# Kernel tuning notes

Hardware: AMD Instinct MI355X
Metric: run time of the kernel (lower is better)

Reference implementation:

```python
import jax, jax.numpy as jnp
import numpy as np

N_HEADS = 16
D_HEAD = 64
IGNORE = -100000.0


def setup_inputs() -> dict:
    key = jax.random.key(0)
    ks = jax.random.split(key, 5)
    B, S, D = 2, 2048, 1024
    return {
        "residual": jax.random.normal(ks[0], (B, S, D), dtype=jnp.float32),
        "q": jax.random.normal(ks[1], (B, S, D), dtype=jnp.float32),
        "k": jax.random.normal(ks[2], (B, S, D), dtype=jnp.float32),
        "v": jax.random.normal(ks[3], (B, S, D), dtype=jnp.float32),
        "W_O": jax.random.normal(ks[4], (N_HEADS, D_HEAD, D), dtype=jnp.float32) * 0.02,
        "b_O": jnp.zeros((D,), dtype=jnp.float32),
    }


def reference(residual, q, k, v, W_O, b_O):
    B, S, _ = q.shape
    attn_scale = np.sqrt(D_HEAD).astype(np.float32)  # use_attn_scale=True
    # split heads: [..., pos, (h d)] -> [..., pos, h, d]
    qh = q.reshape(B, S, N_HEADS, D_HEAD)
    kh = k.reshape(B, S, N_HEADS, D_HEAD)
    vh = v.reshape(B, S, N_HEADS, D_HEAD)
    # scores: [..., head, query_pos, key_pos]
    scores = jnp.einsum("bqhd,bkhd->bhqk", qh, kh) / attn_scale
    causal = jnp.tril(jnp.ones((S, S), dtype=bool))
    scores = jnp.where(causal, scores, jnp.float32(IGNORE))
    pattern = jax.nn.softmax(scores, axis=-1)
    # weighted sum of values: [..., query_pos, head, d_head]
    z = jnp.einsum("bkhd,bhqk->bqhd", vh, pattern)
    out = jnp.einsum("bqhd,hdm->bqm", z, W_O) + b_O
    return (residual, out)
```

## Files before the change

kernel.cpp:

```cpp
#include <hip/hip_runtime.h>

#define B_ 2
#define S_ 2048
#define D_ 1024
#define H_ 16
#define DH_ 64
#define NP_ 2048

typedef short v8s __attribute__((ext_vector_type(8)));
typedef float v4f __attribute__((ext_vector_type(4)));
typedef float v16f __attribute__((ext_vector_type(16)));
typedef unsigned int v2u __attribute__((ext_vector_type(2)));
typedef unsigned int v4u __attribute__((ext_vector_type(4)));
typedef unsigned int uint32;

__device__ inline short f2bf(float f) {
  unsigned u = __float_as_uint(f);
  u = (u + 0x7FFFu + ((u >> 16) & 1u)) >> 16;
  return (short)u;
}

__device__ inline unsigned pk_bf16(float lo, float hi) {
  unsigned r;
  asm("v_cvt_pk_bf16_f32 %0, %1, %2" : "=v"(r) : "v"(lo), "v"(hi));
  return r;
}

__device__ inline void gll16(const void* g, void* l) {
  __builtin_amdgcn_global_load_lds(
      (const __attribute__((address_space(1))) void*)g,
      (__attribute__((address_space(3))) void*)l, 16, 0, 0);
}

__global__ __launch_bounds__(256) void cvt_bf16_kernel(const float* __restrict__ in,
                                                       short* __restrict__ out) {
  int i = blockIdx.x * blockDim.x + threadIdx.x;
  float4 a = ((const float4*)in)[2 * i];
  float4 b = ((const float4*)in)[2 * i + 1];
  v8s t;
  t[0] = f2bf(a.x); t[1] = f2bf(a.y); t[2] = f2bf(a.z); t[3] = f2bf(a.w);
  t[4] = f2bf(b.x); t[5] = f2bf(b.y); t[6] = f2bf(b.z); t[7] = f2bf(b.w);
  ((v8s*)out)[i] = t;
}

__global__ __launch_bounds__(256) void cvt_vt_kernel(const float* __restrict__ v,
                                                     short* __restrict__ vt) {
  int bid = blockIdx.x;
  int st = bid & 31;
  int bh = bid >> 5;
  int b = bh >> 4, h = bh & 15;
  int tid = threadIdx.x;
  __shared__ short t[64][64 + 8];
  int r = tid >> 2, c16 = (tid & 3) * 16;
  const float* vp = v + ((size_t)(b * S_ + st * 64 + r)) * D_ + h * DH_ + c16;
  for (int i = 0; i < 16; i += 4) {
    float4 a = *(const float4*)(vp + i);
    t[r][c16 + i + 0] = f2bf(a.x);
    t[r][c16 + i + 1] = f2bf(a.y);
    t[r][c16 + i + 2] = f2bf(a.z);
    t[r][c16 + i + 3] = f2bf(a.w);
  }
  __syncthreads();
  short* op = vt + ((size_t)((b * H_ + h) * DH_ + r)) * S_ + st * 64 + c16;
  v8s o0, o1;
  for (int j = 0; j < 8; ++j) { o0[j] = t[c16 + j][r]; o1[j] = t[c16 + 8 + j][r]; }
  *(v8s*)op = o0;
  *(v8s*)(op + 8) = o1;
}

__global__ __launch_bounds__(256) void cvt_wt_kernel(const float* __restrict__ w,
                                                     short* __restrict__ wt) {
  int bid = blockIdx.x;
  int tk = bid & 15, tm = bid >> 4;
  int tid = threadIdx.x;
  __shared__ short t[64][64 + 8];
  int r = tid >> 2, c16 = (tid & 3) * 16;
  const float* wp = w + (size_t)(tk * 64 + r) * D_ + tm * 64 + c16;
  for (int i = 0; i < 16; i += 4) {
    float4 a = *(const float4*)(wp + i);
    t[r][c16 + i + 0] = f2bf(a.x);
    t[r][c16 + i + 1] = f2bf(a.y);
    t[r][c16 + i + 2] = f2bf(a.z);
    t[r][c16 + i + 3] = f2bf(a.w);
  }
  __syncthreads();
  short* op = wt + (size_t)(tm * 64 + r) * D_ + tk * 64 + c16;
  v8s o0, o1;
  for (int j = 0; j < 8; ++j) { o0[j] = t[c16 + j][r]; o1[j] = t[c16 + 8 + j][r]; }
  *(v8s*)op = o0;
  *(v8s*)(op + 8) = o1;
}

template <int SPLITS>
__global__ __launch_bounds__(128, 4) void attn_kernel(
    const float* __restrict__ q, const short* __restrict__ kbf,
    const short* __restrict__ vtb, uint32* __restrict__ Opart,
    float* __restrict__ Lsum) {
  constexpr int SHIFT = (SPLITS == 2 ? 6 : 5);
  int bid = blockIdx.x;
  int bh = bid & 31;
  int sp = (SPLITS == 2) ? ((bid >> 5) & 1) : 0;
  int qt = 31 - (int)(bid >> SHIFT);
  int b = bh >> 4, h = bh & 15;

  int nt = qt + 1;
  int hs = (nt + 1) >> 1;
  int t0 = (SPLITS == 2 && sp == 1) ? hs : 0;
  int t1 = (SPLITS == 2 && sp == 0) ? hs - 1 : qt;

  int tid = threadIdx.x;
  int wave = tid >> 6, lane = tid & 63;
  int l31 = lane & 31, h32 = lane >> 5;

  __shared__ short Klds[64][64];
  __shared__ short Vlds[64][64];

  const int qrow0 = qt * 64 + wave * 32;
  const int lr8 = lane >> 3;
  const int scol = ((lane & 7) ^ lr8) << 3;

  const short* pk_ = kbf + (size_t)b * S_ * D_ + h * DH_ +
                     (size_t)(t0 * 64 + wave * 8 + lr8) * D_ + scol;
  const short* pv_ = vtb + (size_t)(b * H_ + h) * DH_ * S_ +
                     (size_t)(wave * 8 + lr8) * S_ + t0 * 64 + scol;

  v8s qf[4];
  {
    const float* qp = q + (size_t)(b * S_ + qrow0 + l31) * D_ + h * DH_ + h32 * 8;
    const float sc = 0.125f * 1.44269504f;
#pragma unroll
    for (int d4 = 0; d4 < 4; ++d4) {
      float4 x = *(const float4*)(qp + d4 * 16);
      float4 y = *(const float4*)(qp + d4 * 16 + 4);
      v8s tq;
      tq[0] = f2bf(x.x * sc); tq[1] = f2bf(x.y * sc);
      tq[2] = f2bf(x.z * sc); tq[3] = f2bf(x.w * sc);
      tq[4] = f2bf(y.x * sc); tq[5] = f2bf(y.y * sc);
      tq[6] = f2bf(y.z * sc); tq[7] = f2bf(y.w * sc);
      qf[d4] = tq;
    }
  }

  v16f O0, O1;
#pragma unroll
  for (int r = 0; r < 16; ++r) { O0[r] = 0.f; O1[r] = 0.f; }
  float L = 0.f;
  const int swz = (l31 & 7) << 3;

  for (int s = t0; s <= t1; ++s) {
#pragma unroll
    for (int i = 0; i < 4; ++i)
      gll16(pk_ + (size_t)(i * 16) * D_, &Klds[i * 16 + wave * 8][0]);
#pragma unroll
    for (int i = 0; i < 4; ++i)
      gll16(pv_ + (size_t)(i * 16) * S_, &Vlds[i * 16 + wave * 8][0]);
    pk_ += (size_t)64 * D_;
    pv_ += 64;
    asm volatile("s_waitcnt vmcnt(0)" ::: "memory");
    __builtin_amdgcn_sched_barrier(0);
    __builtin_amdgcn_s_barrier();
    __builtin_amdgcn_sched_barrier(0);

    int kb = s * 64;
    bool skip1 = (kb >= qrow0);
    bool msk = (kb + 63 > qrow0);

    __builtin_amdgcn_s_setprio(1);
    v16f S0, S1;
#pragma unroll
    for (int r = 0; r < 16; ++r) { S0[r] = 0.f; S1[r] = 0.f; }
#pragma unroll
    for (int d4 = 0; d4 < 4; ++d4) {
      v8s kf = *(const v8s*)&Klds[l31][(((d4 << 1) | h32) << 3) ^ swz];
      S0 = __builtin_amdgcn_mfma_f32_32x32x16_bf16(kf, qf[d4], S0, 0, 0, 0);
    }
    if (!skip1) {
#pragma unroll
      for (int d4 = 0; d4 < 4; ++d4) {
        v8s kf = *(const v8s*)&Klds[32 + l31][(((d4 << 1) | h32) << 3) ^ swz];
        S1 = __builtin_amdgcn_mfma_f32_32x32x16_bf16(kf, qf[d4], S1, 0, 0, 0);
      }
    }
    __builtin_amdgcn_s_setprio(0);

    int qg = qrow0 + l31;
    if (msk) {
#pragma unroll
      for (int r = 0; r < 16; ++r) {
        int kl = kb + (r & 3) + 8 * (r >> 2) + 4 * h32;
        if (kl > qg) S0[r] = -1e30f;
      }
      if (!skip1) {
#pragma unroll
        for (int r = 0; r < 16; ++r) {
          int kl = kb + 32 + (r & 3) + 8 * (r >> 2) + 4 * h32;
          if (kl > qg) S1[r] = -1e30f;
        }
      }
    }

    float rs = 0.f;
    unsigned pw0[8], pw1[8];
#pragma unroll
    for (int r = 0; r < 16; ++r) {
      S0[r] = __builtin_amdgcn_exp2f(S0[r]);
      rs += S0[r];
    }
#pragma unroll
    for (int w = 0; w < 8; ++w) pw0[w] = pk_bf16(S0[2 * w], S0[2 * w + 1]);
    if (!skip1) {
#pragma unroll
      for (int r = 0; r < 16; ++r) {
        S1[r] = __builtin_amdgcn_exp2f(S1[r]);
        rs += S1[r];
      }
#pragma unroll
      for (int w = 0; w < 8; ++w) pw1[w] = pk_bf16(S1[2 * w], S1[2 * w + 1]);
    }
    rs += __shfl_xor(rs, 32);
    L += rs;

    __builtin_amdgcn_s_setprio(1);
#pragma unroll
    for (int ks = 0; ks < 2; ++ks) {
      v2u a = __builtin_amdgcn_permlane32_swap(pw0[ks * 4 + 0], pw0[ks * 4 + 2], false, false);
      v2u c = __builtin_amdgcn_permlane32_swap(pw0[ks * 4 + 1], pw0[ks * 4 + 3], false, false);
      v4u fw; fw.x = a.x; fw.y = c.x; fw.z = a.y; fw.w = c.y;
      v8s pb = __builtin_bit_cast(v8s, fw);
      v8s vf0 = *(const v8s*)&Vlds[l31][(((ks << 1) | h32) << 3) ^ swz];
      O0 = __builtin_amdgcn_mfma_f32_32x32x16_bf16(vf0, pb, O0, 0, 0, 0);
      v8s vf1 = *(const v8s*)&Vlds[32 + l31][(((ks << 1) | h32) << 3) ^ swz];
      O1 = __builtin_amdgcn_mfma_f32_32x32x16_bf16(vf1, pb, O1, 0, 0, 0);
    }
    if (!skip1) {
#pragma unroll
      for (int ks = 0; ks < 2; ++ks) {
        v2u a = __builtin_amdgcn_permlane32_swap(pw1[ks * 4 + 0], pw1[ks * 4 + 2], false, false);
        v2u c = __builtin_amdgcn_permlane32_swap(pw1[ks * 4 + 1], pw1[ks * 4 + 3], false, false);
        v4u fw; fw.x = a.x; fw.y = c.x; fw.z = a.y; fw.w = c.y;
        v8s pb = __builtin_bit_cast(v8s, fw);
        v8s vf0 = *(const v8s*)&Vlds[l31][((((ks + 2) << 1) | h32) << 3) ^ swz];
        O0 = __builtin_amdgcn_mfma_f32_32x32x16_bf16(vf0, pb, O0, 0, 0, 0);
        v8s vf1 = *(const v8s*)&Vlds[32 + l31][((((ks + 2) << 1) | h32) << 3) ^ swz];
        O1 = __builtin_amdgcn_mfma_f32_32x32x16_bf16(vf1, pb, O1, 0, 0, 0);
      }
    }
    __builtin_amdgcn_s_setprio(0);

    __builtin_amdgcn_sched_barrier(0);
    __builtin_amdgcn_s_barrier();
    __builtin_amdgcn_sched_barrier(0);
  }

  int p = bh * 64 + qt * 2 + wave;
  uint32* Op = Opart + ((size_t)(sp * NP_ + p)) * 1024;
#pragma unroll
  for (int w = 0; w < 8; ++w) {
    int dpair = 4 * (w >> 1) + (w & 1) + 2 * h32;
    Op[dpair * 32 + l31] = pk_bf16(O0[2 * w], O0[2 * w + 1]);
    Op[(16 + dpair) * 32 + l31] = pk_bf16(O1[2 * w], O1[2 * w + 1]);
  }
  if (h32 == 0) Lsum[(size_t)(sp * NP_ + p) * 32 + l31] = L;
}

template <int SPLITS>
__global__ __launch_bounds__(128) void merge_kernel(
    const uint32* __restrict__ Opart, const float* __restrict__ Lsum,
    short* __restrict__ z) {
  int p = blockIdx.x;
  int tid = threadIdx.x;
  int qq = tid & 31, g = tid >> 5;

  float Lt = Lsum[(size_t)p * 32 + qq];
  if constexpr (SPLITS == 2) Lt += Lsum[(size_t)(NP_ + p) * 32 + qq];
  float f = 1.f / Lt;

  __shared__ uint32 T[32][33];
  const uint32* O0 = Opart + (size_t)p * 1024;
  const uint32* O1 = Opart + (size_t)(NP_ + p) * 1024;
#pragma unroll
  for (int j = 0; j < 8; ++j) {
    int dp = g * 8 + j;
    uint32 u0 = O0[dp * 32 + qq];
    float lo = __uint_as_float(u0 << 16);
    float hi = __uint_as_float(u0 & 0xFFFF0000u);
    if constexpr (SPLITS == 2) {
      uint32 u1 = O1[dp * 32 + qq];
      lo += __uint_as_float(u1 << 16);
      hi += __uint_as_float(u1 & 0xFFFF0000u);
    }
    T[qq][dp] = pk_bf16(lo * f, hi * f);
  }
  __syncthreads();
  int q2 = tid >> 2, c = (tid & 3) * 8;
  int srow = (p & 63) * 32 + q2;
  int b = p >> 10, h = (p >> 6) & 15;
  uint32* zp = (uint32*)z + ((size_t)(b * S_ + srow)) * (D_ / 2) + h * 32 + c;
#pragma unroll
  for (int j = 0; j < 8; ++j) zp[j] = T[q2][c + j];
}

__global__ __launch_bounds__(256) void proj_kernel(
    const short* __restrict__ z, const short* __restrict__ wt,
    const float* __restrict__ bias, float* __restrict__ out) {
  int bm = blockIdx.x, bn = blockIdx.y;
  int tid = threadIdx.x;
  int wave = tid >> 6, lane = tid & 63, lh = lane >> 4, ll = lane & 15;
  int wr = wave >> 1, wc = wave & 1;

  __shared__ short Al[2][64][64];
  __shared__ short Bl[2][128][64];

  const int r8 = lane >> 3;
  const int scol = ((lane & 7) ^ r8) << 3;

  v4f acc[2][4];
#pragma unroll
  for (int m = 0; m < 2; ++m)
#pragma unroll
    for (int n = 0; n < 4; ++n) acc[m][n] = (v4f){0.f, 0.f, 0.f, 0.f};

  auto stage = [&](int kb, int bbuf) {
#pragma unroll
    for (int i = 0; i < 2; ++i) {
      int c = wave * 2 + i;
      gll16(z + (size_t)(bm * 64 + c * 8 + r8) * D_ + kb + scol, &Al[bbuf][c * 8][0]);
    }
#pragma unroll
    for (int i = 0; i < 4; ++i) {
      int c = wave * 4 + i;
      gll16(wt + (size_t)(bn * 128 + c * 8 + r8) * D_ + kb + scol, &Bl[bbuf][c * 8][0]);
    }
  };

  stage(0, 0);
  __syncthreads();

  for (int kt = 0; kt < D_ / 64; ++kt) {
    int bbuf = kt & 1;
    if (kt + 1 < D_ / 64) stage((kt + 1) * 64, bbuf ^ 1);
    v8s af[2][2], bf[4][2];
#pragma unroll
    for (int m = 0; m < 2; ++m) {
      int row = wr * 32 + m * 16 + ll;
#pragma unroll
      for (int c = 0; c < 2; ++c)
        af[m][c] = *(const v8s*)&Al[bbuf][row][(((c << 2) | lh) ^ (ll & 7)) << 3];
    }
#pragma unroll
    for (int n = 0; n < 4; ++n) {
      int row = wc * 64 + n * 16 + ll;
#pragma unroll
      for (int c = 0; c < 2; ++c)
        bf[n][c] = *(const v8s*)&Bl[bbuf][row][(((c << 2) | lh) ^ (ll & 7)) << 3];
    }
#pragma unroll
    for (int m = 0; m < 2; ++m)
#pragma unroll
      for (int n = 0; n < 4; ++n)
#pragma unroll
        for (int c = 0; c < 2; ++c)
          acc[m][n] = __builtin_amdgcn_mfma_f32_16x16x32_bf16(af[m][c], bf[n][c], acc[m][n], 0, 0, 0);
    __syncthreads();
  }

#pragma unroll
  for (int m = 0; m < 2; ++m) {
    int gr = bm * 64 + wr * 32 + m * 16 + lh * 4;
#pragma unroll
    for (int n = 0; n < 4; ++n) {
      int gc = bn * 128 + wc * 64 + n * 16 + ll;
      float bo = bias[gc];
#pragma unroll
      for (int r = 0; r < 4; ++r)
        out[(size_t)(gr + r) * D_ + gc] = acc[m][n][r] + bo;
    }
  }
}

extern "C" void kernel_launch(void* const* d_in, const int* in_sizes, int n_in,
                              void* d_out, int out_size, void* d_ws, size_t ws_size,
                              hipStream_t stream) {
  const float* residual = (const float*)d_in[0];
  const float* q = (const float*)d_in[1];
  const float* k = (const float*)d_in[2];
  const float* v = (const float*)d_in[3];
  const float* W = (const float*)d_in[4];
  const float* bO = (const float*)d_in[5];
  float* out = (float*)d_out;

  const size_t half = (size_t)B_ * S_ * D_;
  char* ws = (char*)d_ws;
  short* z = (short*)ws;
  short* kbf = z + half;
  short* vtb = kbf + half;
  short* wtb = vtb + half;
  char* pbase = (char*)(wtb + (size_t)D_ * D_);
  const size_t opart_b = (size_t)NP_ * 1024 * 4;
  const size_t l_b = (size_t)NP_ * 32 * 4;
  const size_t base_b = (size_t)pbase - (size_t)ws;

  hipMemcpyAsync(out, residual, half * sizeof(float), hipMemcpyDeviceToDevice, stream);

  cvt_bf16_kernel<<<half / 2048, 256, 0, stream>>>(k, kbf);
  cvt_vt_kernel<<<B_ * H_ * (S_ / 64), 256, 0, stream>>>(v, vtb);
  cvt_wt_kernel<<<(D_ / 64) * (D_ / 64), 256, 0, stream>>>(W, wtb);

  if (ws_size >= base_b + 2 * (opart_b + l_b)) {
    uint32* Opart = (uint32*)pbase;
    float* Lsum = (float*)(pbase + 2 * opart_b);
    attn_kernel<2><<<2048, 128, 0, stream>>>(q, kbf, vtb, Opart, Lsum);
    merge_kernel<2><<<NP_, 128, 0, stream>>>(Opart, Lsum, z);
  } else {
    uint32* Opart = (uint32*)pbase;
    float* Lsum = (float*)(pbase + opart_b);
    attn_kernel<1><<<1024, 128, 0, stream>>>(q, kbf, vtb, Opart, Lsum);
    merge_kernel<1><<<NP_, 128, 0, stream>>>(Opart, Lsum, z);
  }

  proj_kernel<<<dim3((B_ * S_) / 64, D_ / 128), 256, 0, stream>>>(z, wtb, bO, out + half);
}
```

Before: 77.09 us.

## Fuse conversions, balance causal split-K by tile length, fold residual copy into attention

Merges the three bf16 conversion kernels into one launch. Splits causal query tiles into 1–4 key chunks depending on tile length, so every attention block handles a similar amount of work, and the merge reduces a variable number of partials. Moves the residual memcpy into the tail of the attention kernel as a grid-stride copy, and reuses the K buffer for z to save workspace. This cuts launch count and tail imbalance, but adds more partial-buffer traffic and workspace.

```diff
diff --git a/kernel.cpp b/kernel.cpp
--- a/kernel.cpp
+++ b/kernel.cpp
@@ -32,81 +32,88 @@
       (__attribute__((address_space(3))) void*)l, 16, 0, 0);
 }
 
-__global__ __launch_bounds__(256) void cvt_bf16_kernel(const float* __restrict__ in,
-                                                       short* __restrict__ out) {
-  int i = blockIdx.x * blockDim.x + threadIdx.x;
-  float4 a = ((const float4*)in)[2 * i];
-  float4 b = ((const float4*)in)[2 * i + 1];
-  v8s t;
-  t[0] = f2bf(a.x); t[1] = f2bf(a.y); t[2] = f2bf(a.z); t[3] = f2bf(a.w);
-  t[4] = f2bf(b.x); t[5] = f2bf(b.y); t[6] = f2bf(b.z); t[7] = f2bf(b.w);
-  ((v8s*)out)[i] = t;
-}
-
-__global__ __launch_bounds__(256) void cvt_vt_kernel(const float* __restrict__ v,
-                                                     short* __restrict__ vt) {
+__global__ __launch_bounds__(256) void cvt_all_kernel(
+    const float* __restrict__ k, short* __restrict__ kb,
+    const float* __restrict__ v, short* __restrict__ vt,
+    const float* __restrict__ w, short* __restrict__ wt) {
+  __shared__ short t[64][64 + 8];
   int bid = blockIdx.x;
-  int st = bid & 31;
-  int bh = bid >> 5;
-  int b = bh >> 4, h = bh & 15;
   int tid = threadIdx.x;
-  __shared__ short t[64][64 + 8];
+  if (bid < 2048) {
+    int i = bid * 256 + tid;
+    float4 a = ((const float4*)k)[2 * i];
+    float4 b = ((const float4*)k)[2 * i + 1];
+    v8s o;
+    o[0] = f2bf(a.x); o[1] = f2bf(a.y); o[2] = f2bf(a.z); o[3] = f2bf(a.w);
+    o[4] = f2bf(b.x); o[5] = f2bf(b.y); o[6] = f2bf(b.z); o[7] = f2bf(b.w);
+    ((v8s*)kb)[i] = o;
+    return;
+  }
   int r = tid >> 2, c16 = (tid & 3) * 16;
-  const float* vp = v + ((size_t)(b * S_ + st * 64 + r)) * D_ + h * DH_ + c16;
-  for (int i = 0; i < 16; i += 4) {
-    float4 a = *(const float4*)(vp + i);
-    t[r][c16 + i + 0] = f2bf(a.x);
-    t[r][c16 + i + 1] = f2bf(a.y);
-    t[r][c16 + i + 2] = f2bf(a.z);
-    t[r][c16 + i + 3] = f2bf(a.w);
-  }
-  __syncthreads();
-  short* op = vt + ((size_t)((b * H_ + h) * DH_ + r)) * S_ + st * 64 + c16;
-  v8s o0, o1;
-  for (int j = 0; j < 8; ++j) { o0[j] = t[c16 + j][r]; o1[j] = t[c16 + 8 + j][r]; }
-  *(v8s*)op = o0;
-  *(v8s*)(op + 8) = o1;
-}
-
-__global__ __launch_bounds__(256) void cvt_wt_kernel(const float* __restrict__ w,
-                                                     short* __restrict__ wt) {
-  int bid = blockIdx.x;
-  int tk = bid & 15, tm = bid >> 4;
-  int tid = threadIdx.x;
-  __shared__ short t[64][64 + 8];
-  int r = tid >> 2, c16 = (tid & 3) * 16;
-  const float* wp = w + (size_t)(tk * 64 + r) * D_ + tm * 64 + c16;
-  for (int i = 0; i < 16; i += 4) {
-    float4 a = *(const float4*)(wp + i);
-    t[r][c16 + i + 0] = f2bf(a.x);
-    t[r][c16 + i + 1] = f2bf(a.y);
-    t[r][c16 + i + 2] = f2bf(a.z);
-    t[r][c16 + i + 3] = f2bf(a.w);
-  }
-  __syncthreads();
-  short* op = wt + (size_t)(tm * 64 + r) * D_ + tk * 64 + c16;
-  v8s o0, o1;
-  for (int j = 0; j < 8; ++j) { o0[j] = t[c16 + j][r]; o1[j] = t[c16 + 8 + j][r]; }
-  *(v8s*)op = o0;
-  *(v8s*)(op + 8) = o1;
-}
-
-template <int SPLITS>
+  if (bid < 3072) {
+    int id = bid - 2048;
+    int st = id & 31;
+    int bh = id >> 5;
+    int b = bh >> 4, h = bh & 15;
+    const float* vp = v + ((size_t)(b * S_ + st * 64 + r)) * D_ + h * DH_ + c16;
+    for (int i = 0; i < 16; i += 4) {
+      float4 a = *(const float4*)(vp + i);
+      t[r][c16 + i + 0] = f2bf(a.x);
+      t[r][c16 + i + 1] = f2bf(a.y);
+      t[r][c16 + i + 2] = f2bf(a.z);
+      t[r][c16 + i + 3] = f2bf(a.w);
+    }
+    __syncthreads();
+    short* op = vt + ((size_t)((b * H_ + h) * DH_ + r)) * S_ + st * 64 + c16;
+    v8s o0, o1;
+    for (int j = 0; j < 8; ++j) { o0[j] = t[c16 + j][r]; o1[j] = t[c16 + 8 + j][r]; }
+    *(v8s*)op = o0;
+    *(v8s*)(op + 8) = o1;
+  } else {
+    int id = bid - 3072;
+    int tk = id & 15, tm = id >> 4;
+    const float* wp = w + (size_t)(tk * 64 + r) * D_ + tm * 64 + c16;
+    for (int i = 0; i < 16; i += 4) {
+      float4 a = *(const float4*)(wp + i);
+      t[r][c16 + i + 0] = f2bf(a.x);
+      t[r][c16 + i + 1] = f2bf(a.y);
+      t[r][c16 + i + 2] = f2bf(a.z);
+      t[r][c16 + i + 3] = f2bf(a.w);
+    }
+    __syncthreads();
+    short* op = wt + (size_t)(tm * 64 + r) * D_ + tk * 64 + c16;
+    v8s o0, o1;
+    for (int j = 0; j < 8; ++j) { o0[j] = t[c16 + j][r]; o1[j] = t[c16 + 8 + j][r]; }
+    *(v8s*)op = o0;
+    *(v8s*)(op + 8) = o1;
+  }
+}
+
+template <int MAXSP>
 __global__ __launch_bounds__(128, 4) void attn_kernel(
     const float* __restrict__ q, const short* __restrict__ kbf,
     const short* __restrict__ vtb, uint32* __restrict__ Opart,
-    float* __restrict__ Lsum) {
-  constexpr int SHIFT = (SPLITS == 2 ? 6 : 5);
+    float* __restrict__ Lsum, const float* __restrict__ residual,
+    float* __restrict__ res_out) {
+  constexpr int NBLK = (MAXSP == 4) ? 2560 : 1536;
   int bid = blockIdx.x;
   int bh = bid & 31;
-  int sp = (SPLITS == 2) ? ((bid >> 5) & 1) : 0;
-  int qt = 31 - (int)(bid >> SHIFT);
+  int sidx = bid >> 5;
+  int qt, sp;
+  if constexpr (MAXSP == 4) {
+    if (sidx < 32) { qt = 31 - (sidx >> 2); sp = sidx & 3; }
+    else if (sidx < 56) { int t = sidx - 32; qt = 23 - t / 3; sp = t % 3; }
+    else if (sidx < 72) { int t = sidx - 56; qt = 15 - ((t) >> 1); sp = t & 1; }
+    else { qt = 7 - (sidx - 72); sp = 0; }
+  } else {
+    if (sidx < 32) { qt = 31 - (sidx >> 1); sp = sidx & 1; }
+    else { qt = 15 - (sidx - 32); sp = 0; }
+  }
+  const int ns = qt / (32 / MAXSP) + 1;
+  const int nt = qt + 1;
+  const int t0 = sp * nt / ns;
+  const int t1 = (sp + 1) * nt / ns - 1;
   int b = bh >> 4, h = bh & 15;
-
-  int nt = qt + 1;
-  int hs = (nt + 1) >> 1;
-  int t0 = (SPLITS == 2 && sp == 1) ? hs : 0;
-  int t1 = (SPLITS == 2 && sp == 0) ? hs - 1 : qt;
 
   int tid = threadIdx.x;
   int wave = tid >> 6, lane = tid & 63;
@@ -119,10 +126,10 @@
   const int lr8 = lane >> 3;
   const int scol = ((lane & 7) ^ lr8) << 3;
 
-  const short* pk_ = kbf + (size_t)b * S_ * D_ + h * DH_ +
-                     (size_t)(t0 * 64 + wave * 8 + lr8) * D_ + scol;
-  const short* pv_ = vtb + (size_t)(b * H_ + h) * DH_ * S_ +
-                     (size_t)(wave * 8 + lr8) * S_ + t0 * 64 + scol;
+  const short* kbase = kbf + (size_t)b * S_ * D_ + h * DH_ +
+                       (size_t)(wave * 8 + lr8) * D_ + scol;
+  const short* vbase = vtb + (size_t)(b * H_ + h) * DH_ * S_ +
+                       (size_t)(wave * 8 + lr8) * S_ + scol;
 
   v8s qf[4];
   {
@@ -148,14 +155,16 @@
   const int swz = (l31 & 7) << 3;
 
   for (int s = t0; s <= t1; ++s) {
-#pragma unroll
-    for (int i = 0; i < 4; ++i)
-      gll16(pk_ + (size_t)(i * 16) * D_, &Klds[i * 16 + wave * 8][0]);
-#pragma unroll
-    for (int i = 0; i < 4; ++i)
-      gll16(pv_ + (size_t)(i * 16) * S_, &Vlds[i * 16 + wave * 8][0]);
-    pk_ += (size_t)64 * D_;
-    pv_ += 64;
+    {
+      const short* kp = kbase + (size_t)(s * 64) * D_;
+      const short* vp = vbase + s * 64;
+#pragma unroll
+      for (int i = 0; i < 4; ++i)
+        gll16(kp + (size_t)(i * 16) * D_, &Klds[i * 16 + wave * 8][0]);
+#pragma unroll
+      for (int i = 0; i < 4; ++i)
+        gll16(vp + (size_t)(i * 16) * S_, &Vlds[i * 16 + wave * 8][0]);
+    }
     asm volatile("s_waitcnt vmcnt(0)" ::: "memory");
     __builtin_amdgcn_sched_barrier(0);
     __builtin_amdgcn_s_barrier();
@@ -261,34 +270,44 @@
     Op[(16 + dpair) * 32 + l31] = pk_bf16(O1[2 * w], O1[2 * w + 1]);
   }
   if (h32 == 0) Lsum[(size_t)(sp * NP_ + p) * 32 + l31] = L;
-}
-
-template <int SPLITS>
+
+  {
+    const float4* rs_ = (const float4*)residual;
+    float4* rd_ = (float4*)res_out;
+    const int total = NBLK * 128;
+    for (size_t i = (size_t)bid * 128 + tid; i < 1048576; i += total)
+      rd_[i] = rs_[i];
+  }
+}
+
+template <int MAXSP>
 __global__ __launch_bounds__(128) void merge_kernel(
     const uint32* __restrict__ Opart, const float* __restrict__ Lsum,
     short* __restrict__ z) {
   int p = blockIdx.x;
+  int qt = (p >> 1) & 31;
+  const int ns = qt / (32 / MAXSP) + 1;
   int tid = threadIdx.x;
   int qq = tid & 31, g = tid >> 5;
 
-  float Lt = Lsum[(size_t)p * 32 + qq];
-  if constexpr (SPLITS == 2) Lt += Lsum[(size_t)(NP_ + p) * 32 + qq];
+  float Lt = 0.f;
+#pragma unroll
+  for (int sp = 0; sp < MAXSP; ++sp)
+    if (sp < ns) Lt += Lsum[((size_t)sp * NP_ + p) * 32 + qq];
   float f = 1.f / Lt;
 
   __shared__ uint32 T[32][33];
-  const uint32* O0 = Opart + (size_t)p * 1024;
-  const uint32* O1 = Opart + (size_t)(NP_ + p) * 1024;
 #pragma unroll
   for (int j = 0; j < 8; ++j) {
     int dp = g * 8 + j;
-    uint32 u0 = O0[dp * 32 + qq];
-    float lo = __uint_as_float(u0 << 16);
-    float hi = __uint_as_float(u0 & 0xFFFF0000u);
-    if constexpr (SPLITS == 2) {
-      uint32 u1 = O1[dp * 32 + qq];
-      lo += __uint_as_float(u1 << 16);
-      hi += __uint_as_float(u1 & 0xFFFF0000u);
-    }
+    float lo = 0.f, hi = 0.f;
+#pragma unroll
+    for (int sp = 0; sp < MAXSP; ++sp)
+      if (sp < ns) {
+        uint32 u = Opart[((size_t)sp * NP_ + p) * 1024 + dp * 32 + qq];
+        lo += __uint_as_float(u << 16);
+        hi += __uint_as_float(u & 0xFFFF0000u);
+      }
     T[qq][dp] = pk_bf16(lo * f, hi * f);
   }
   __syncthreads();
@@ -391,32 +410,28 @@
 
   const size_t half = (size_t)B_ * S_ * D_;
   char* ws = (char*)d_ws;
-  short* z = (short*)ws;
-  short* kbf = z + half;
+  short* kbf = (short*)ws;
   short* vtb = kbf + half;
   short* wtb = vtb + half;
   char* pbase = (char*)(wtb + (size_t)D_ * D_);
   const size_t opart_b = (size_t)NP_ * 1024 * 4;
   const size_t l_b = (size_t)NP_ * 32 * 4;
   const size_t base_b = (size_t)pbase - (size_t)ws;
-
-  hipMemcpyAsync(out, residual, half * sizeof(float), hipMemcpyDeviceToDevice, stream);
-
-  cvt_bf16_kernel<<<half / 2048, 256, 0, stream>>>(k, kbf);
-  cvt_vt_kernel<<<B_ * H_ * (S_ / 64), 256, 0, stream>>>(v, vtb);
-  cvt_wt_kernel<<<(D_ / 64) * (D_ / 64), 256, 0, stream>>>(W, wtb);
-
-  if (ws_size >= base_b + 2 * (opart_b + l_b)) {
+  short* z = kbf;
+
+  cvt_all_kernel<<<3328, 256, 0, stream>>>(k, kbf, v, vtb, W, wtb);
+
+  if (ws_size >= base_b + 4 * (opart_b + l_b)) {
+    uint32* Opart = (uint32*)pbase;
+    float* Lsum = (float*)(pbase + 4 * opart_b);
+    attn_kernel<4><<<2560, 128, 0, stream>>>(q, kbf, vtb, Opart, Lsum, residual, out);
+    merge_kernel<4><<<NP_, 128, 0, stream>>>(Opart, Lsum, z);
+    proj_kernel<<<dim3((B_ * S_) / 64, D_ / 128), 256, 0, stream>>>(z, wtb, bO, out + half);
+  } else {
     uint32* Opart = (uint32*)pbase;
     float* Lsum = (float*)(pbase + 2 * opart_b);
-    attn_kernel<2><<<2048, 128, 0, stream>>>(q, kbf, vtb, Opart, Lsum);
+    attn_kernel<2><<<1536, 128, 0, stream>>>(q, kbf, vtb, Opart, Lsum, residual, out);
     merge_kernel<2><<<NP_, 128, 0, stream>>>(Opart, Lsum, z);
-  } else {
-    uint32* Opart = (uint32*)pbase;
-    float* Lsum = (float*)(pbase + opart_b);
-    attn_kernel<1><<<1024, 128, 0, stream>>>(q, kbf, vtb, Opart, Lsum);
-    merge_kernel<1><<<NP_, 128, 0, stream>>>(Opart, Lsum, z);
-  }
-
-  proj_kernel<<<dim3((B_ * S_) / 64, D_ / 128), 256, 0, stream>>>(z, wtb, bO, out + half);
-}
+    proj_kernel<<<dim3((B_ * S_) / 64, D_ / 128), 256, 0, stream>>>(z, wtb, bO, out + half);
+  }
+}
```

Result: slower. 81.76 us (+6.0%).

## Fuse conversion kernels, fold residual copy into attention, enlarge projection tiles

Applied to the files above, without the earlier changes.

The three bf16 conversion kernels are merged into one launch that dispatches on block index. The residual device-to-device memcpy is removed and each attention block now copies a slice of the residual to the output at its end. The projection GEMM moves from 64x128 to 128x128 tiles on a flat 256-block grid, and z now reuses the kbf workspace buffer. The goal is fewer launches and less per-launch overhead, at the cost of extra tail work in attention and fewer, heavier projection blocks (256 blocks on a large GPU), which may lower occupancy.

```diff
diff --git a/kernel.cpp b/kernel.cpp
--- a/kernel.cpp
+++ b/kernel.cpp
@@ -32,70 +32,69 @@
       (__attribute__((address_space(3))) void*)l, 16, 0, 0);
 }
 
-__global__ __launch_bounds__(256) void cvt_bf16_kernel(const float* __restrict__ in,
-                                                       short* __restrict__ out) {
-  int i = blockIdx.x * blockDim.x + threadIdx.x;
-  float4 a = ((const float4*)in)[2 * i];
-  float4 b = ((const float4*)in)[2 * i + 1];
-  v8s t;
-  t[0] = f2bf(a.x); t[1] = f2bf(a.y); t[2] = f2bf(a.z); t[3] = f2bf(a.w);
-  t[4] = f2bf(b.x); t[5] = f2bf(b.y); t[6] = f2bf(b.z); t[7] = f2bf(b.w);
-  ((v8s*)out)[i] = t;
-}
-
-__global__ __launch_bounds__(256) void cvt_vt_kernel(const float* __restrict__ v,
-                                                     short* __restrict__ vt) {
+__global__ __launch_bounds__(256) void cvt_all_kernel(
+    const float* __restrict__ k, short* __restrict__ kb,
+    const float* __restrict__ v, short* __restrict__ vt,
+    const float* __restrict__ w, short* __restrict__ wt) {
+  __shared__ short t[64][64 + 8];
   int bid = blockIdx.x;
-  int st = bid & 31;
-  int bh = bid >> 5;
-  int b = bh >> 4, h = bh & 15;
   int tid = threadIdx.x;
-  __shared__ short t[64][64 + 8];
+  if (bid < 2048) {
+    int i = bid * 256 + tid;
+    float4 a = ((const float4*)k)[2 * i];
+    float4 b = ((const float4*)k)[2 * i + 1];
+    v8s o;
+    o[0] = f2bf(a.x); o[1] = f2bf(a.y); o[2] = f2bf(a.z); o[3] = f2bf(a.w);
+    o[4] = f2bf(b.x); o[5] = f2bf(b.y); o[6] = f2bf(b.z); o[7] = f2bf(b.w);
+    ((v8s*)kb)[i] = o;
+    return;
+  }
   int r = tid >> 2, c16 = (tid & 3) * 16;
-  const float* vp = v + ((size_t)(b * S_ + st * 64 + r)) * D_ + h * DH_ + c16;
-  for (int i = 0; i < 16; i += 4) {
-    float4 a = *(const float4*)(vp + i);
-    t[r][c16 + i + 0] = f2bf(a.x);
-    t[r][c16 + i + 1] = f2bf(a.y);
-    t[r][c16 + i + 2] = f2bf(a.z);
-    t[r][c16 + i + 3] = f2bf(a.w);
-  }
-  __syncthreads();
-  short* op = vt + ((size_t)((b * H_ + h) * DH_ + r)) * S_ + st * 64 + c16;
-  v8s o0, o1;
-  for (int j = 0; j < 8; ++j) { o0[j] = t[c16 + j][r]; o1[j] = t[c16 + 8 + j][r]; }
-  *(v8s*)op = o0;
-  *(v8s*)(op + 8) = o1;
-}
-
-__global__ __launch_bounds__(256) void cvt_wt_kernel(const float* __restrict__ w,
-                                                     short* __restrict__ wt) {
-  int bid = blockIdx.x;
-  int tk = bid & 15, tm = bid >> 4;
-  int tid = threadIdx.x;
-  __shared__ short t[64][64 + 8];
-  int r = tid >> 2, c16 = (tid & 3) * 16;
-  const float* wp = w + (size_t)(tk * 64 + r) * D_ + tm * 64 + c16;
-  for (int i = 0; i < 16; i += 4) {
-    float4 a = *(const float4*)(wp + i);
-    t[r][c16 + i + 0] = f2bf(a.x);
-    t[r][c16 + i + 1] = f2bf(a.y);
-    t[r][c16 + i + 2] = f2bf(a.z);
-    t[r][c16 + i + 3] = f2bf(a.w);
-  }
-  __syncthreads();
-  short* op = wt + (size_t)(tm * 64 + r) * D_ + tk * 64 + c16;
-  v8s o0, o1;
-  for (int j = 0; j < 8; ++j) { o0[j] = t[c16 + j][r]; o1[j] = t[c16 + 8 + j][r]; }
-  *(v8s*)op = o0;
-  *(v8s*)(op + 8) = o1;
+  if (bid < 3072) {
+    int id = bid - 2048;
+    int st = id & 31;
+    int bh = id >> 5;
+    int b = bh >> 4, h = bh & 15;
+    const float* vp = v + ((size_t)(b * S_ + st * 64 + r)) * D_ + h * DH_ + c16;
+    for (int i = 0; i < 16; i += 4) {
+      float4 a = *(const float4*)(vp + i);
+      t[r][c16 + i + 0] = f2bf(a.x);
+      t[r][c16 + i + 1] = f2bf(a.y);
+      t[r][c16 + i + 2] = f2bf(a.z);
+      t[r][c16 + i + 3] = f2bf(a.w);
+    }
+    __syncthreads();
+    short* op = vt + ((size_t)((b * H_ + h) * DH_ + r)) * S_ + st * 64 + c16;
+    v8s o0, o1;
+    for (int j = 0; j < 8; ++j) { o0[j] = t[c16 + j][r]; o1[j] = t[c16 + 8 + j][r]; }
+    *(v8s*)op = o0;
+    *(v8s*)(op + 8) = o1;
+  } else {
+    int id = bid - 3072;
+    int tk = id & 15, tm = id >> 4;
+    const float* wp = w + (size_t)(tk * 64 + r) * D_ + tm * 64 + c16;
+    for (int i = 0; i < 16; i += 4) {
+      float4 a = *(const float4*)(wp + i);
+      t[r][c16 + i + 0] = f2bf(a.x);
+      t[r][c16 + i + 1] = f2bf(a.y);
+      t[r][c16 + i + 2] = f2bf(a.z);
+      t[r][c16 + i + 3] = f2bf(a.w);
+    }
+    __syncthreads();
+    short* op = wt + (size_t)(tm * 64 + r) * D_ + tk * 64 + c16;
+    v8s o0, o1;
+    for (int j = 0; j < 8; ++j) { o0[j] = t[c16 + j][r]; o1[j] = t[c16 + 8 + j][r]; }
+    *(v8s*)op = o0;
+    *(v8s*)(op + 8) = o1;
+  }
 }
 
 template <int SPLITS>
 __global__ __launch_bounds__(128, 4) void attn_kernel(
     const float* __restrict__ q, const short* __restrict__ kbf,
     const short* __restrict__ vtb, uint32* __restrict__ Opart,
-    float* __restrict__ Lsum) {
+    float* __restrict__ Lsum, const float* __restrict__ residual,
+    float* __restrict__ res_out) {
   constexpr int SHIFT = (SPLITS == 2 ? 6 : 5);
   int bid = blockIdx.x;
   int bh = bid & 31;
@@ -261,6 +260,15 @@
     Op[(16 + dpair) * 32 + l31] = pk_bf16(O1[2 * w], O1[2 * w + 1]);
   }
   if (h32 == 0) Lsum[(size_t)(sp * NP_ + p) * 32 + l31] = L;
+
+  {
+    constexpr int F4 = (SPLITS == 2) ? 4 : 8;
+    const float4* rs_ = (const float4*)residual;
+    float4* rd_ = (float4*)res_out;
+    size_t base = (size_t)bid * (128 * F4) + tid;
+#pragma unroll
+    for (int j = 0; j < F4; ++j) rd_[base + j * 128] = rs_[base + j * 128];
+  }
 }
 
 template <int SPLITS>
@@ -272,20 +280,18 @@
   int qq = tid & 31, g = tid >> 5;
 
   float Lt = Lsum[(size_t)p * 32 + qq];
-  if constexpr (SPLITS == 2) Lt += Lsum[(size_t)(NP_ + p) * 32 + qq];
+  if constexpr (SPLITS == 2) Lt += Lsum[((size_t)NP_ + p) * 32 + qq];
   float f = 1.f / Lt;
 
   __shared__ uint32 T[32][33];
-  const uint32* O0 = Opart + (size_t)p * 1024;
-  const uint32* O1 = Opart + (size_t)(NP_ + p) * 1024;
 #pragma unroll
   for (int j = 0; j < 8; ++j) {
     int dp = g * 8 + j;
-    uint32 u0 = O0[dp * 32 + qq];
+    uint32 u0 = Opart[(size_t)p * 1024 + dp * 32 + qq];
     float lo = __uint_as_float(u0 << 16);
     float hi = __uint_as_float(u0 & 0xFFFF0000u);
     if constexpr (SPLITS == 2) {
-      uint32 u1 = O1[dp * 32 + qq];
+      uint32 u1 = Opart[((size_t)NP_ + p) * 1024 + dp * 32 + qq];
       lo += __uint_as_float(u1 << 16);
       hi += __uint_as_float(u1 & 0xFFFF0000u);
     }
@@ -303,28 +309,29 @@
 __global__ __launch_bounds__(256) void proj_kernel(
     const short* __restrict__ z, const short* __restrict__ wt,
     const float* __restrict__ bias, float* __restrict__ out) {
-  int bm = blockIdx.x, bn = blockIdx.y;
+  int bid = blockIdx.x;
+  int bm = bid & 31, bn = bid >> 5;
   int tid = threadIdx.x;
   int wave = tid >> 6, lane = tid & 63, lh = lane >> 4, ll = lane & 15;
   int wr = wave >> 1, wc = wave & 1;
 
-  __shared__ short Al[2][64][64];
+  __shared__ short Al[2][128][64];
   __shared__ short Bl[2][128][64];
 
   const int r8 = lane >> 3;
   const int scol = ((lane & 7) ^ r8) << 3;
 
-  v4f acc[2][4];
-#pragma unroll
-  for (int m = 0; m < 2; ++m)
+  v4f acc[4][4];
+#pragma unroll
+  for (int m = 0; m < 4; ++m)
 #pragma unroll
     for (int n = 0; n < 4; ++n) acc[m][n] = (v4f){0.f, 0.f, 0.f, 0.f};
 
   auto stage = [&](int kb, int bbuf) {
 #pragma unroll
-    for (int i = 0; i < 2; ++i) {
-      int c = wave * 2 + i;
-      gll16(z + (size_t)(bm * 64 + c * 8 + r8) * D_ + kb + scol, &Al[bbuf][c * 8][0]);
+    for (int i = 0; i < 4; ++i) {
+      int c = wave * 4 + i;
+      gll16(z + (size_t)(bm * 128 + c * 8 + r8) * D_ + kb + scol, &Al[bbuf][c * 8][0]);
     }
 #pragma unroll
     for (int i = 0; i < 4; ++i) {
@@ -339,10 +346,10 @@
   for (int kt = 0; kt < D_ / 64; ++kt) {
     int bbuf = kt & 1;
     if (kt + 1 < D_ / 64) stage((kt + 1) * 64, bbuf ^ 1);
-    v8s af[2][2], bf[4][2];
-#pragma unroll
-    for (int m = 0; m < 2; ++m) {
-      int row = wr * 32 + m * 16 + ll;
+    v8s af[4][2], bf[4][2];
+#pragma unroll
+    for (int m = 0; m < 4; ++m) {
+      int row = wr * 64 + m * 16 + ll;
 #pragma unroll
       for (int c = 0; c < 2; ++c)
         af[m][c] = *(const v8s*)&Al[bbuf][row][(((c << 2) | lh) ^ (ll & 7)) << 3];
@@ -355,7 +362,7 @@
         bf[n][c] = *(const v8s*)&Bl[bbuf][row][(((c << 2) | lh) ^ (ll & 7)) << 3];
     }
 #pragma unroll
-    for (int m = 0; m < 2; ++m)
+    for (int m = 0; m < 4; ++m)
 #pragma unroll
       for (int n = 0; n < 4; ++n)
 #pragma unroll
@@ -365,8 +372,8 @@
   }
 
 #pragma unroll
-  for (int m = 0; m < 2; ++m) {
-    int gr = bm * 64 + wr * 32 + m * 16 + lh * 4;
+  for (int m = 0; m < 4; ++m) {
+    int gr = bm * 128 + wr * 64 + m * 16 + lh * 4;
 #pragma unroll
     for (int n = 0; n < 4; ++n) {
       int gc = bn * 128 + wc * 64 + n * 16 + ll;
@@ -391,32 +398,27 @@
 
   const size_t half = (size_t)B_ * S_ * D_;
   char* ws = (char*)d_ws;
-  short* z = (short*)ws;
-  short* kbf = z + half;
+  short* kbf = (short*)ws;
   short* vtb = kbf + half;
   short* wtb = vtb + half;
   char* pbase = (char*)(wtb + (size_t)D_ * D_);
   const size_t opart_b = (size_t)NP_ * 1024 * 4;
   const size_t l_b = (size_t)NP_ * 32 * 4;
   const size_t base_b = (size_t)pbase - (size_t)ws;
-
-  hipMemcpyAsync(out, residual, half * sizeof(float), hipMemcpyDeviceToDevice, stream);
-
-  cvt_bf16_kernel<<<half / 2048, 256, 0, stream>>>(k, kbf);
-  cvt_vt_kernel<<<B_ * H_ * (S_ / 64), 256, 0, stream>>>(v, vtb);
-  cvt_wt_kernel<<<(D_ / 64) * (D_ / 64), 256, 0, stream>>>(W, wtb);
+  short* z = kbf;
+
+  cvt_all_kernel<<<3328, 256, 0, stream>>>(k, kbf, v, vtb, W, wtb);
 
   if (ws_size >= base_b + 2 * (opart_b + l_b)) {
     uint32* Opart = (uint32*)pbase;
     float* Lsum = (float*)(pbase + 2 * opart_b);
-    attn_kernel<2><<<2048, 128, 0, stream>>>(q, kbf, vtb, Opart, Lsum);
+    attn_kernel<2><<<2048, 128, 0, stream>>>(q, kbf, vtb, Opart, Lsum, residual, out);
     merge_kernel<2><<<NP_, 128, 0, stream>>>(Opart, Lsum, z);
   } else {
     uint32* Opart = (uint32*)pbase;
     float* Lsum = (float*)(pbase + opart_b);
-    attn_kernel<1><<<1024, 128, 0, stream>>>(q, kbf, vtb, Opart, Lsum);
+    attn_kernel<1><<<1024, 128, 0, stream>>>(q, kbf, vtb, Opart, Lsum, residual, out);
     merge_kernel<1><<<NP_, 128, 0, stream>>>(Opart, Lsum, z);
   }
-
-  proj_kernel<<<dim3((B_ * S_) / 64, D_ / 128), 256, 0, stream>>>(z, wtb, bO, out + half);
-}
+  proj_kernel<<<256, 256, 0, stream>>>(z, wtb, bO, out + half);
+}
```

Result: faster. 74.11 us (-3.9%).
